# Kernel tuning notes

Measured on AMD Instinct MI355X. Metric: run time of the kernel, lower is better.

The kernel has to match this reference:

```python
import jax, jax.numpy as jnp
import numpy as np

OBS_DIM = 64
HID = 1440
K = HID // 90
N_ORN, N_PN, N_LN, N_KC, N_MBON = 24 * K, 7 * K, 4 * K, 54 * K, 1 * K
B, T, INNER = 256, 128, 4


def _lin_w(key, out_d, in_d):
    bound = 1.0 / np.sqrt(in_d)
    return jax.random.uniform(key, (out_d, in_d), jnp.float32, -bound, bound)


def setup_inputs() -> dict:
    key = jax.random.key(0)
    ks = jax.random.split(key, 20)
    return {
        "obs": jax.random.normal(ks[0], (B, T, OBS_DIM), jnp.float32),
        "h": jnp.zeros((B, HID), jnp.float32),
        "in_orn_w": _lin_w(ks[1], N_ORN, OBS_DIM),
        "in_orn_b": jnp.zeros((N_ORN,), jnp.float32),
        "W_oto": _lin_w(ks[2], N_ORN, N_ORN),
        "W_lto": _lin_w(ks[3], N_ORN, N_LN),
        "W_otp": _lin_w(ks[4], N_PN, N_ORN),
        "W_ltp": _lin_w(ks[5], N_PN, N_LN),
        "W_ptp": _lin_w(ks[6], N_PN, N_PN),
        "W_otl": _lin_w(ks[7], N_LN, N_ORN),
        "W_ptl": _lin_w(ks[8], N_LN, N_PN),
        "W_ltl": _lin_w(ks[9], N_LN, N_LN),
        "W_ktk": _lin_w(ks[10], N_KC, N_KC),
        "W_mtk": _lin_w(ks[11], N_KC, N_MBON),
        "W_ptk": _lin_w(ks[12], N_KC, N_PN),
        "W_ktm": _lin_w(ks[13], N_MBON, N_KC),
        "b_orn": jnp.zeros((N_ORN,), jnp.float32),
        "b_pn": jnp.zeros((N_PN,), jnp.float32),
        "b_ln": jnp.zeros((N_LN,), jnp.float32),
        "b_kc": jnp.zeros((N_KC,), jnp.float32),
        "b_mbon": jnp.zeros((N_MBON,), jnp.float32),
        "readout_w": _lin_w(ks[14], HID, N_MBON),
        "readout_b": jnp.zeros((HID,), jnp.float32),
    }


def reference(obs, h, in_orn_w, in_orn_b, W_oto, W_lto, W_otp, W_ltp, W_ptp,
              W_otl, W_ptl, W_ltl, W_ktk, W_mtk, W_ptk, W_ktm,
              b_orn, b_pn, b_ln, b_kc, b_mbon, readout_w, readout_b):
    # split packed hidden state into the five populations
    i0, i1, i2, i3 = N_ORN, N_ORN + N_PN, N_ORN + N_PN + N_LN, N_ORN + N_PN + N_LN + N_KC
    carry0 = (h[:, :i0], h[:, i0:i1], h[:, i1:i2], h[:, i2:i3], h[:, i3:])

    def step(h_orn, h_pn, h_ln, h_kc, h_mbon, x_t):
        orn = jnp.tanh(h_orn @ W_oto.T + h_ln @ W_lto.T + x_t + b_orn)
        pn = jnp.tanh(orn @ W_otp.T + h_ln @ W_ltp.T + h_pn @ W_ptp.T + b_pn)
        ln = jnp.tanh(orn @ W_otl.T + pn @ W_ptl.T + h_ln @ W_ltl.T + b_ln)
        kc = jnp.tanh(h_kc @ W_ktk.T + h_mbon @ W_mtk.T + pn @ W_ptk.T + b_kc)
        mbon = jnp.tanh(kc @ W_ktm.T + b_mbon)
        return orn, pn, ln, kc, mbon

    def scan_fn(carry, obs_t):  # obs_t: [B, OBS_DIM]
        x_t = obs_t @ in_orn_w.T + in_orn_b  # [B, N_ORN]
        h_orn, h_pn, h_ln, h_kc, h_mbon = carry
        for _ in range(INNER):  # fixed small inner recurrence
            h_orn, h_pn, h_ln, h_kc, h_mbon = step(h_orn, h_pn, h_ln, h_kc, h_mbon, x_t)
        y_t = h_mbon @ readout_w.T + readout_b  # [B, HID]
        return (h_orn, h_pn, h_ln, h_kc, h_mbon), y_t

    carry, ys = jax.lax.scan(scan_fn, carry0, jnp.swapaxes(obs, 0, 1))
    y = jnp.swapaxes(ys, 0, 1)  # [B, T, HID]
    h2 = jnp.concatenate(carry, axis=-1)[None]  # [1, B, HID]
    return y, h2
```

## Files before the change

kernel.cpp:

```cpp
#include <hip/hip_runtime.h>
#include <hip/hip_fp16.h>
#include <hip/hip_cooperative_groups.h>

namespace cg = cooperative_groups;

#define NTHREADS 1024
#define BT 16

constexpr int Bsz = 256, Tst = 128, HID = 1440;
constexpr int ORN = 384, PN = 112, LN = 64, KC = 864, MB = 16, OBS = 64;
constexpr int WO = 448;
constexpr int WP = 576;
constexpr int WK = 992;
constexpr int WL = 560;

struct Params {
  const float *obs, *h, *in_orn_w, *in_orn_b, *W_oto, *W_lto, *W_otp, *W_ltp, *W_ptp,
              *W_otl, *W_ptl, *W_ltl, *W_ktk, *W_mtk, *W_ptk, *W_ktm,
              *b_orn, *b_pn, *b_ln, *b_kc, *b_mbon, *readout_w, *readout_b;
  float *orn0, *orn1, *pn0, *pn1, *ln0, *ln1, *kc0, *kc1, *mbon, *y, *h2;
  __half *Wp_orn, *Wp_pn, *Wp_kc, *Wp_ln, *Wh_ktm, *Wh_ro;
  int *bar;
};

template <int K>
__device__ __forceinline__ float dot4(const float* __restrict__ w, const float* __restrict__ a) {
  const float4* w4 = (const float4*)w;
  const float4* a4 = (const float4*)a;
  float x0 = 0.f, x1 = 0.f, x2 = 0.f, x3 = 0.f;
#pragma unroll 4
  for (int i = 0; i < K / 4; ++i) {
    float4 wv = w4[i], av = a4[i];
    x0 = fmaf(wv.x, av.x, x0); x1 = fmaf(wv.y, av.y, x1);
    x2 = fmaf(wv.z, av.z, x2); x3 = fmaf(wv.w, av.w, x3);
  }
  return (x0 + x1) + (x2 + x3);
}

template <int K>
__device__ __forceinline__ float doth(const __half* __restrict__ w, const float* __restrict__ a) {
  const float4* w4 = (const float4*)w;
  const float4* a4 = (const float4*)a;
  float x0 = 0.f, x1 = 0.f, x2 = 0.f, x3 = 0.f;
#pragma unroll 4
  for (int i = 0; i < K / 8; ++i) {
    float4 wv = w4[i];
    float4 a0 = a4[2 * i], a1 = a4[2 * i + 1];
    __half2 h0 = __builtin_bit_cast(__half2, wv.x);
    __half2 h1 = __builtin_bit_cast(__half2, wv.y);
    __half2 h2 = __builtin_bit_cast(__half2, wv.z);
    __half2 h3 = __builtin_bit_cast(__half2, wv.w);
    x0 = fmaf(__low2float(h0), a0.x, x0); x1 = fmaf(__high2float(h0), a0.y, x1);
    x2 = fmaf(__low2float(h1), a0.z, x2); x3 = fmaf(__high2float(h1), a0.w, x3);
    x0 = fmaf(__low2float(h2), a1.x, x0); x1 = fmaf(__high2float(h2), a1.y, x1);
    x2 = fmaf(__low2float(h3), a1.z, x2); x3 = fmaf(__high2float(h3), a1.w, x3);
  }
  return (x0 + x1) + (x2 + x3);
}

__device__ __forceinline__ void load_seg(float* dst, int stride, int off,
                                         const float* g, int width, int b0, int tid) {
  int w4 = width >> 2;
  const float4* g4 = (const float4*)(g + (size_t)b0 * width);
  for (int idx = tid; idx < BT * w4; idx += NTHREADS) {
    int b = idx / w4, k = idx - b * w4;
    *(float4*)(dst + b * stride + off + 4 * k) = g4[(size_t)b * w4 + k];
  }
}

__device__ __forceinline__ void st_h2(__half* p, float v0, float v1) {
  __half2 h = __floats2half2_rn(v0, v1);
  __hip_atomic_store((unsigned*)p, __builtin_bit_cast(unsigned, h),
                     __ATOMIC_RELAXED, __HIP_MEMORY_SCOPE_AGENT);
}

__device__ __forceinline__ void bar_sync(int* cnt, int* gen, int& lg, int tid) {
  __syncthreads();
  if (tid == 0) {
    int target = ++lg;
    asm volatile("s_waitcnt vmcnt(0)" ::: "memory");
    int old = __hip_atomic_fetch_add(cnt, 1, __ATOMIC_RELAXED, __HIP_MEMORY_SCOPE_AGENT);
    if (old == 15) {
      __hip_atomic_store(cnt, 0, __ATOMIC_RELAXED, __HIP_MEMORY_SCOPE_AGENT);
      asm volatile("s_waitcnt vmcnt(0)" ::: "memory");
      __hip_atomic_fetch_add(gen, 1, __ATOMIC_RELAXED, __HIP_MEMORY_SCOPE_AGENT);
    } else {
      while (__hip_atomic_load(gen, __ATOMIC_RELAXED, __HIP_MEMORY_SCOPE_AGENT) < target)
        __builtin_amdgcn_s_sleep(1);
    }
    asm volatile("buffer_inv sc0\n\ts_waitcnt vmcnt(0)" ::: "memory");
  }
  __syncthreads();
}

__global__ void __launch_bounds__(NTHREADS, 4)
conn_kernel(Params P) {
  cg::grid_group grid = cg::this_grid();
  __shared__ float act[BT * 996];
  __shared__ float xs[BT * 24];
  const int tid = threadIdx.x;
  const int wg = blockIdx.x;
  const int bg = wg & 15, ng = wg >> 4, b0 = bg * BT;
  int* cnt = P.bar + bg * 64;
  int* gen = P.bar + bg * 64 + 16;
  int lg = 0;

  {
    const int gid = wg * NTHREADS + tid, gstr = 256 * NTHREADS;
    for (int idx = gid; idx < 384 * (WO / 2); idx += gstr) {
      int r = idx / (WO / 2), c = (idx - r * (WO / 2)) * 2;
      float v0, v1;
      if (c < 384) { v0 = P.W_oto[(size_t)r * 384 + c]; v1 = P.W_oto[(size_t)r * 384 + c + 1]; }
      else         { v0 = P.W_lto[(size_t)r * 64 + c - 384]; v1 = P.W_lto[(size_t)r * 64 + c - 383]; }
      st_h2(&P.Wp_orn[(size_t)r * WO + c], v0, v1);
    }
    for (int idx = gid; idx < 112 * (WP / 2); idx += gstr) {
      int r = idx / (WP / 2), c = (idx - r * (WP / 2)) * 2;
      float v0, v1;
      if      (c < 384) { v0 = P.W_otp[(size_t)r * 384 + c];     v1 = P.W_otp[(size_t)r * 384 + c + 1]; }
      else if (c < 448) { v0 = P.W_ltp[(size_t)r * 64 + c - 384]; v1 = P.W_ltp[(size_t)r * 64 + c - 383]; }
      else if (c < 560) { v0 = P.W_ptp[(size_t)r * 112 + c - 448]; v1 = P.W_ptp[(size_t)r * 112 + c - 447]; }
      else              { v0 = 0.f; v1 = 0.f; }
      st_h2(&P.Wp_pn[(size_t)r * WP + c], v0, v1);
    }
    for (int idx = gid; idx < 864 * (WK / 2); idx += gstr) {
      int r = idx / (WK / 2), c = (idx - r * (WK / 2)) * 2;
      float v0, v1;
      if      (c < 864) { v0 = P.W_ktk[(size_t)r * 864 + c];      v1 = P.W_ktk[(size_t)r * 864 + c + 1]; }
      else if (c < 976) { v0 = P.W_ptk[(size_t)r * 112 + c - 864]; v1 = P.W_ptk[(size_t)r * 112 + c - 863]; }
      else              { v0 = P.W_mtk[(size_t)r * 16 + c - 976];  v1 = P.W_mtk[(size_t)r * 16 + c - 975]; }
      st_h2(&P.Wp_kc[(size_t)r * WK + c], v0, v1);
    }
    for (int idx = gid; idx < 64 * (WL / 2); idx += gstr) {
      int r = idx / (WL / 2), c = (idx - r * (WL / 2)) * 2;
      float v0, v1;
      if      (c < 384) { v0 = P.W_otl[(size_t)r * 384 + c];      v1 = P.W_otl[(size_t)r * 384 + c + 1]; }
      else if (c < 496) { v0 = P.W_ptl[(size_t)r * 112 + c - 384]; v1 = P.W_ptl[(size_t)r * 112 + c - 383]; }
      else              { v0 = P.W_ltl[(size_t)r * 64 + c - 496];  v1 = P.W_ltl[(size_t)r * 64 + c - 495]; }
      st_h2(&P.Wp_ln[(size_t)r * WL + c], v0, v1);
    }
    for (int idx = gid; idx < 16 * 432; idx += gstr) {
      int c = idx * 2;
      st_h2(&P.Wh_ktm[c], P.W_ktm[c], P.W_ktm[c + 1]);
    }
    for (int idx = gid; idx < 1440 * 8; idx += gstr) {
      int c = idx * 2;
      st_h2(&P.Wh_ro[c], P.readout_w[c], P.readout_w[c + 1]);
    }
  }

  if (ng == 0) {
    if (tid == 0) { *cnt = 0; *gen = 0; }
    for (int idx = tid; idx < BT * HID; idx += NTHREADS) {
      int b = idx / HID, pos = idx - b * HID, gb = b0 + b;
      float v = P.h[(size_t)gb * HID + pos];
      if      (pos < 384)  P.orn1[(size_t)gb * ORN + pos] = v;
      else if (pos < 496)  P.pn1[gb * PN + (pos - 384)] = v;
      else if (pos < 560)  P.ln1[gb * LN + (pos - 496)] = v;
      else if (pos < 1424) P.kc1[(size_t)gb * KC + (pos - 560)] = v;
      else                 P.mbon[gb * MB + (pos - 1424)] = v;
    }
  }
  grid.sync();

  for (int s = 0; s < Tst * 4; ++s) {
    const int t = s >> 2, i = s & 3, p = s & 1;
    float* ornN = p ? P.orn1 : P.orn0;  const float* ornO = p ? P.orn0 : P.orn1;
    float* pnN  = p ? P.pn1  : P.pn0;   const float* pnO  = p ? P.pn0  : P.pn1;
    float* lnN  = p ? P.ln1  : P.ln0;   const float* lnO  = p ? P.ln0  : P.ln1;
    float* kcN  = p ? P.kc1  : P.kc0;   const float* kcO  = p ? P.kc0  : P.kc1;

    load_seg(act, 996, 0,   ornO, ORN, b0, tid);
    load_seg(act, 996, 384, lnO,  LN,  b0, tid);
    if (i == 0 && tid >= 640) {
      for (int o = tid - 640; o < BT * 24; o += 384) {
        int b = o / 24, jl = o - b * 24, j = ng * 24 + jl;
        xs[b * 24 + jl] = P.in_orn_b[j]
          + dot4<OBS>(P.in_orn_w + (size_t)j * OBS,
                      P.obs + ((size_t)(b0 + b) * Tst + t) * OBS);
      }
    }
    __syncthreads();
    if (tid < 384) {
      int b = tid & 15, j = tid >> 4, jg = ng * 24 + j;
      float r = xs[b * 24 + j] + P.b_orn[jg]
              + doth<WO>(P.Wp_orn + (size_t)jg * WO, act + b * 996);
      ornN[(size_t)(b0 + b) * ORN + jg] = tanhf(r);
    } else if (tid >= 448 && tid < 512 && s > 0) {
      int idx = tid - 448, b = idx >> 2, ks = idx & 3;
      float part = doth<216>(P.Wh_ktm + (size_t)ng * KC + ks * 216,
                             kcO + (size_t)(b0 + b) * KC + ks * 216);
      part += __shfl_xor(part, 1);
      part += __shfl_xor(part, 2);
      if (ks == 0)
        P.mbon[(b0 + b) * MB + ng] = tanhf(part + P.b_mbon[ng]);
    }
    bar_sync(cnt, gen, lg, tid);

    load_seg(act, 996, 0,   ornN, ORN, b0, tid);
    load_seg(act, 996, 384, lnO,  LN,  b0, tid);
    load_seg(act, 996, 448, pnO,  PN,  b0, tid);
    for (int idx = tid; idx < BT * 4; idx += NTHREADS) {
      int b = idx >> 2, k = idx & 3;
      *(float4*)(act + b * 996 + 560 + 4 * k) = make_float4(0.f, 0.f, 0.f, 0.f);
    }
    __syncthreads();
    if (tid < 448) {
      int b = tid & 15, ks = (tid >> 4) & 3, j = tid >> 6, jg = ng * 7 + j;
      float r = doth<144>(P.Wp_pn + (size_t)jg * WP + ks * 144,
                          act + b * 996 + ks * 144);
      r += __shfl_xor(r, 16);
      r += __shfl_xor(r, 32);
      if (ks == 0)
        pnN[(size_t)(b0 + b) * PN + jg] = tanhf(r + P.b_pn[jg]);
    } else if (i == 0 && s > 0 && tid >= 512) {
      for (int o = tid - 512; o < BT * 90; o += 512) {
        int b = o / 90, jl = o - b * 90, j = ng * 90 + jl;
        float yv = P.readout_b[j]
          + doth<MB>(P.Wh_ro + (size_t)j * MB, P.mbon + (size_t)(b0 + b) * MB);
        P.y[((size_t)(b0 + b) * Tst + (t - 1)) * HID + j] = yv;
      }
    }
    bar_sync(cnt, gen, lg, tid);

    load_seg(act, 996, 0,   kcO,    KC, b0, tid);
    load_seg(act, 996, 864, pnN,    PN, b0, tid);
    load_seg(act, 996, 976, P.mbon, MB, b0, tid);
    __syncthreads();
    if (tid < 864) {
      int b = tid & 15, j = tid >> 4, jg = ng * 54 + j;
      float r = P.b_kc[jg] + doth<WK>(P.Wp_kc + (size_t)jg * WK, act + b * 996);
      kcN[(size_t)(b0 + b) * KC + jg] = tanhf(r);
    } else if (tid >= 896 && tid < 960) {
      int l = tid - 896, b = l & 15, j = l >> 4, jg = ng * 4 + j;
      const __half* row = P.Wp_ln + (size_t)jg * WL;
      float r = P.b_ln[jg]
        + doth<384>(row,       ornN + (size_t)(b0 + b) * ORN)
        + doth<112>(row + 384, act + b * 996 + 864)
        + doth<64> (row + 496, lnO + (size_t)(b0 + b) * LN);
      lnN[(size_t)(b0 + b) * LN + jg] = tanhf(r);
    }
    bar_sync(cnt, gen, lg, tid);
  }

  if (tid < 64) {
    int b = tid >> 2, ks = tid & 3;
    float part = doth<216>(P.Wh_ktm + (size_t)ng * KC + ks * 216,
                           P.kc1 + (size_t)(b0 + b) * KC + ks * 216);
    part += __shfl_xor(part, 1);
    part += __shfl_xor(part, 2);
    if (ks == 0)
      P.mbon[(b0 + b) * MB + ng] = tanhf(part + P.b_mbon[ng]);
  }
  bar_sync(cnt, gen, lg, tid);
  for (int o = tid; o < BT * 90; o += NTHREADS) {
    int b = o / 90, jl = o - b * 90, j = ng * 90 + jl;
    float acc = P.readout_b[j]
      + doth<MB>(P.Wh_ro + (size_t)j * MB, P.mbon + (size_t)(b0 + b) * MB);
    P.y[((size_t)(b0 + b) * Tst + (Tst - 1)) * HID + j] = acc;
  }
  for (int idx = tid; idx < BT * 90; idx += NTHREADS) {
    int b = idx / 90, pos = idx - b * 90, gb = b0 + b;
    float v; int hp;
    if      (pos < 24) { v = P.orn1[(size_t)gb * ORN + ng * 24 + pos]; hp = ng * 24 + pos; }
    else if (pos < 31) { int l = pos - 24; v = P.pn1[gb * PN + ng * 7 + l]; hp = 384 + ng * 7 + l; }
    else if (pos < 35) { int l = pos - 31; v = P.ln1[gb * LN + ng * 4 + l]; hp = 496 + ng * 4 + l; }
    else if (pos < 89) { int l = pos - 35; v = P.kc1[(size_t)gb * KC + ng * 54 + l]; hp = 560 + ng * 54 + l; }
    else               { v = P.mbon[gb * MB + ng]; hp = 1424 + ng; }
    P.h2[(size_t)gb * HID + hp] = v;
  }
}

extern "C" void kernel_launch(void* const* d_in, const int* in_sizes, int n_in,
                              void* d_out, int out_size, void* d_ws, size_t ws_size,
                              hipStream_t stream) {
  Params P;
  P.obs       = (const float*)d_in[0];
  P.h         = (const float*)d_in[1];
  P.in_orn_w  = (const float*)d_in[2];
  P.in_orn_b  = (const float*)d_in[3];
  P.W_oto     = (const float*)d_in[4];
  P.W_lto     = (const float*)d_in[5];
  P.W_otp     = (const float*)d_in[6];
  P.W_ltp     = (const float*)d_in[7];
  P.W_ptp     = (const float*)d_in[8];
  P.W_otl     = (const float*)d_in[9];
  P.W_ptl     = (const float*)d_in[10];
  P.W_ltl     = (const float*)d_in[11];
  P.W_ktk     = (const float*)d_in[12];
  P.W_mtk     = (const float*)d_in[13];
  P.W_ptk     = (const float*)d_in[14];
  P.W_ktm     = (const float*)d_in[15];
  P.b_orn     = (const float*)d_in[16];
  P.b_pn      = (const float*)d_in[17];
  P.b_ln      = (const float*)d_in[18];
  P.b_kc      = (const float*)d_in[19];
  P.b_mbon    = (const float*)d_in[20];
  P.readout_w = (const float*)d_in[21];
  P.readout_b = (const float*)d_in[22];

  float* ws = (float*)d_ws;
  size_t off = 0;
  P.orn0 = ws + off; off += (size_t)Bsz * ORN;
  P.orn1 = ws + off; off += (size_t)Bsz * ORN;
  P.pn0  = ws + off; off += (size_t)Bsz * PN;
  P.pn1  = ws + off; off += (size_t)Bsz * PN;
  P.ln0  = ws + off; off += (size_t)Bsz * LN;
  P.ln1  = ws + off; off += (size_t)Bsz * LN;
  P.kc0  = ws + off; off += (size_t)Bsz * KC;
  P.kc1  = ws + off; off += (size_t)Bsz * KC;
  P.mbon = ws + off; off += (size_t)Bsz * MB;
  P.bar  = (int*)(ws + off); off += 16 * 64;
  P.Wp_orn = (__half*)(ws + off); off += (size_t)384 * WO / 2;
  P.Wp_pn  = (__half*)(ws + off); off += (size_t)112 * WP / 2;
  P.Wp_kc  = (__half*)(ws + off); off += (size_t)864 * WK / 2;
  P.Wp_ln  = (__half*)(ws + off); off += (size_t)64  * WL / 2;
  P.Wh_ktm = (__half*)(ws + off); off += (size_t)16  * KC / 2;
  P.Wh_ro  = (__half*)(ws + off); off += (size_t)HID * MB / 2;

  P.y  = (float*)d_out;
  P.h2 = (float*)d_out + (size_t)Bsz * Tst * HID;

  void* args[] = { &P };
  hipLaunchCooperativeKernel((void*)conn_kernel, dim3(256), dim3(NTHREADS), args, 0, stream);
}
```

Baseline: 17.60 ms.

## Store activations in fp16 and use packed fdot2 with two-row dot products

Recurrent state buffers and the shared activation tile move from fp32 to fp16, halving global and LDS traffic for the per-step state exchanges. Dot products switch to the packed v_dot2 f16 instruction, which multiplies two half pairs per instruction with an fp32 accumulator. The ORN and KC stages now compute two output rows per thread so each activation load is reused. The cost is fp16 rounding of the hidden state carried through 512 recurrent steps, which may drift numerically, and fewer active threads per stage.

```diff
diff --git a/kernel.cpp b/kernel.cpp
--- a/kernel.cpp
+++ b/kernel.cpp
@@ -13,15 +13,29 @@
 constexpr int WP = 576;
 constexpr int WK = 992;
 constexpr int WL = 560;
+constexpr int SH = 1032;
 
 struct Params {
   const float *obs, *h, *in_orn_w, *in_orn_b, *W_oto, *W_lto, *W_otp, *W_ltp, *W_ptp,
               *W_otl, *W_ptl, *W_ltl, *W_ktk, *W_mtk, *W_ptk, *W_ktm,
               *b_orn, *b_pn, *b_ln, *b_kc, *b_mbon, *readout_w, *readout_b;
-  float *orn0, *orn1, *pn0, *pn1, *ln0, *ln1, *kc0, *kc1, *mbon, *y, *h2;
+  __half *orn0, *orn1, *pn0, *pn1, *ln0, *ln1, *kc0, *kc1, *mbon;
   __half *Wp_orn, *Wp_pn, *Wp_kc, *Wp_ln, *Wh_ktm, *Wh_ro;
+  float *y, *h2;
   int *bar;
 };
+
+typedef _Float16 hv2 __attribute__((ext_vector_type(2)));
+
+__device__ __forceinline__ float fdot2u(unsigned w, unsigned a, float c) {
+#if __has_builtin(__builtin_amdgcn_fdot2)
+  return __builtin_amdgcn_fdot2(__builtin_bit_cast(hv2, w), __builtin_bit_cast(hv2, a), c, false);
+#else
+  __half2 hw = __builtin_bit_cast(__half2, w), ha = __builtin_bit_cast(__half2, a);
+  c = fmaf(__low2float(hw), __low2float(ha), c);
+  return fmaf(__high2float(hw), __high2float(ha), c);
+#endif
+}
 
 template <int K>
 __device__ __forceinline__ float dot4(const float* __restrict__ w, const float* __restrict__ a) {
@@ -38,33 +52,45 @@
 }
 
 template <int K>
-__device__ __forceinline__ float doth(const __half* __restrict__ w, const float* __restrict__ a) {
-  const float4* w4 = (const float4*)w;
-  const float4* a4 = (const float4*)a;
+__device__ __forceinline__ float doth2(const __half* __restrict__ w, const __half* __restrict__ a) {
+  const uint4* w4 = (const uint4*)w;
+  const uint4* a4 = (const uint4*)a;
   float x0 = 0.f, x1 = 0.f, x2 = 0.f, x3 = 0.f;
 #pragma unroll 4
   for (int i = 0; i < K / 8; ++i) {
-    float4 wv = w4[i];
-    float4 a0 = a4[2 * i], a1 = a4[2 * i + 1];
-    __half2 h0 = __builtin_bit_cast(__half2, wv.x);
-    __half2 h1 = __builtin_bit_cast(__half2, wv.y);
-    __half2 h2 = __builtin_bit_cast(__half2, wv.z);
-    __half2 h3 = __builtin_bit_cast(__half2, wv.w);
-    x0 = fmaf(__low2float(h0), a0.x, x0); x1 = fmaf(__high2float(h0), a0.y, x1);
-    x2 = fmaf(__low2float(h1), a0.z, x2); x3 = fmaf(__high2float(h1), a0.w, x3);
-    x0 = fmaf(__low2float(h2), a1.x, x0); x1 = fmaf(__high2float(h2), a1.y, x1);
-    x2 = fmaf(__low2float(h3), a1.z, x2); x3 = fmaf(__high2float(h3), a1.w, x3);
+    uint4 wv = w4[i], av = a4[i];
+    x0 = fdot2u(wv.x, av.x, x0); x1 = fdot2u(wv.y, av.y, x1);
+    x2 = fdot2u(wv.z, av.z, x2); x3 = fdot2u(wv.w, av.w, x3);
   }
   return (x0 + x1) + (x2 + x3);
 }
 
-__device__ __forceinline__ void load_seg(float* dst, int stride, int off,
-                                         const float* g, int width, int b0, int tid) {
-  int w4 = width >> 2;
-  const float4* g4 = (const float4*)(g + (size_t)b0 * width);
-  for (int idx = tid; idx < BT * w4; idx += NTHREADS) {
-    int b = idx / w4, k = idx - b * w4;
-    *(float4*)(dst + b * stride + off + 4 * k) = g4[(size_t)b * w4 + k];
+template <int K>
+__device__ __forceinline__ void ddoth2(const __half* __restrict__ w0, const __half* __restrict__ w1,
+                                       const __half* __restrict__ a, float& r0, float& r1) {
+  const uint4* W0 = (const uint4*)w0;
+  const uint4* W1 = (const uint4*)w1;
+  const uint4* A  = (const uint4*)a;
+  float x0=0,x1=0,x2=0,x3=0, y0=0,y1=0,y2=0,y3=0;
+#pragma unroll 4
+  for (int i = 0; i < K / 8; ++i) {
+    uint4 av = A[i], u = W0[i], v = W1[i];
+    x0 = fdot2u(u.x, av.x, x0); x1 = fdot2u(u.y, av.y, x1);
+    x2 = fdot2u(u.z, av.z, x2); x3 = fdot2u(u.w, av.w, x3);
+    y0 = fdot2u(v.x, av.x, y0); y1 = fdot2u(v.y, av.y, y1);
+    y2 = fdot2u(v.z, av.z, y2); y3 = fdot2u(v.w, av.w, y3);
+  }
+  r0 += (x0 + x1) + (x2 + x3);
+  r1 += (y0 + y1) + (y2 + y3);
+}
+
+__device__ __forceinline__ void load_seg_h(__half* dst, int offH,
+                                           const __half* g, int widthH, int b0, int tid) {
+  int w8 = widthH >> 3;
+  const uint4* g4 = (const uint4*)(g + (size_t)b0 * widthH);
+  for (int idx = tid; idx < BT * w8; idx += NTHREADS) {
+    int b = idx / w8, k = idx - b * w8;
+    *(uint4*)(dst + b * SH + offH + 8 * k) = g4[(size_t)b * w8 + k];
   }
 }
 
@@ -96,7 +122,7 @@
 __global__ void __launch_bounds__(NTHREADS, 4)
 conn_kernel(Params P) {
   cg::grid_group grid = cg::this_grid();
-  __shared__ float act[BT * 996];
+  __shared__ __align__(16) __half acth[BT * SH];
   __shared__ float xs[BT * 24];
   const int tid = threadIdx.x;
   const int wg = blockIdx.x;
@@ -153,7 +179,7 @@
     if (tid == 0) { *cnt = 0; *gen = 0; }
     for (int idx = tid; idx < BT * HID; idx += NTHREADS) {
       int b = idx / HID, pos = idx - b * HID, gb = b0 + b;
-      float v = P.h[(size_t)gb * HID + pos];
+      __half v = __float2half(P.h[(size_t)gb * HID + pos]);
       if      (pos < 384)  P.orn1[(size_t)gb * ORN + pos] = v;
       else if (pos < 496)  P.pn1[gb * PN + (pos - 384)] = v;
       else if (pos < 560)  P.ln1[gb * LN + (pos - 496)] = v;
@@ -165,13 +191,13 @@
 
   for (int s = 0; s < Tst * 4; ++s) {
     const int t = s >> 2, i = s & 3, p = s & 1;
-    float* ornN = p ? P.orn1 : P.orn0;  const float* ornO = p ? P.orn0 : P.orn1;
-    float* pnN  = p ? P.pn1  : P.pn0;   const float* pnO  = p ? P.pn0  : P.pn1;
-    float* lnN  = p ? P.ln1  : P.ln0;   const float* lnO  = p ? P.ln0  : P.ln1;
-    float* kcN  = p ? P.kc1  : P.kc0;   const float* kcO  = p ? P.kc0  : P.kc1;
-
-    load_seg(act, 996, 0,   ornO, ORN, b0, tid);
-    load_seg(act, 996, 384, lnO,  LN,  b0, tid);
+    __half* ornN = p ? P.orn1 : P.orn0;  const __half* ornO = p ? P.orn0 : P.orn1;
+    __half* pnN  = p ? P.pn1  : P.pn0;   const __half* pnO  = p ? P.pn0  : P.pn1;
+    __half* lnN  = p ? P.ln1  : P.ln0;   const __half* lnO  = p ? P.ln0  : P.ln1;
+    __half* kcN  = p ? P.kc1  : P.kc0;   const __half* kcO  = p ? P.kc0  : P.kc1;
+
+    load_seg_h(acth, 0,   ornO, ORN, b0, tid);
+    load_seg_h(acth, 384, lnO,  LN,  b0, tid);
     if (i == 0 && tid >= 640) {
       for (int o = tid - 640; o < BT * 24; o += 384) {
         int b = o / 24, jl = o - b * 24, j = ng * 24 + jl;
@@ -181,92 +207,98 @@
       }
     }
     __syncthreads();
-    if (tid < 384) {
-      int b = tid & 15, j = tid >> 4, jg = ng * 24 + j;
-      float r = xs[b * 24 + j] + P.b_orn[jg]
-              + doth<WO>(P.Wp_orn + (size_t)jg * WO, act + b * 996);
-      ornN[(size_t)(b0 + b) * ORN + jg] = tanhf(r);
-    } else if (tid >= 448 && tid < 512 && s > 0) {
-      int idx = tid - 448, b = idx >> 2, ks = idx & 3;
-      float part = doth<216>(P.Wh_ktm + (size_t)ng * KC + ks * 216,
-                             kcO + (size_t)(b0 + b) * KC + ks * 216);
+    if (tid < 192) {
+      int b = tid & 15, jp = tid >> 4;
+      int j0 = ng * 24 + 2 * jp, j1 = j0 + 1;
+      float r0 = xs[b * 24 + 2 * jp]     + P.b_orn[j0];
+      float r1 = xs[b * 24 + 2 * jp + 1] + P.b_orn[j1];
+      ddoth2<WO>(P.Wp_orn + (size_t)j0 * WO, P.Wp_orn + (size_t)j1 * WO,
+                 acth + b * SH, r0, r1);
+      *(__half2*)&ornN[(size_t)(b0 + b) * ORN + j0] = __floats2half2_rn(tanhf(r0), tanhf(r1));
+    } else if (tid < 256 && s > 0) {
+      int idx = tid - 192, b = idx >> 2, ks = idx & 3;
+      float part = doth2<216>(P.Wh_ktm + (size_t)ng * KC + ks * 216,
+                              kcO + (size_t)(b0 + b) * KC + ks * 216);
       part += __shfl_xor(part, 1);
       part += __shfl_xor(part, 2);
       if (ks == 0)
-        P.mbon[(b0 + b) * MB + ng] = tanhf(part + P.b_mbon[ng]);
+        P.mbon[(b0 + b) * MB + ng] = __float2half(tanhf(part + P.b_mbon[ng]));
     }
     bar_sync(cnt, gen, lg, tid);
 
-    load_seg(act, 996, 0,   ornN, ORN, b0, tid);
-    load_seg(act, 996, 384, lnO,  LN,  b0, tid);
-    load_seg(act, 996, 448, pnO,  PN,  b0, tid);
-    for (int idx = tid; idx < BT * 4; idx += NTHREADS) {
-      int b = idx >> 2, k = idx & 3;
-      *(float4*)(act + b * 996 + 560 + 4 * k) = make_float4(0.f, 0.f, 0.f, 0.f);
+    load_seg_h(acth, 0,   ornN, ORN, b0, tid);
+    load_seg_h(acth, 384, lnO,  LN,  b0, tid);
+    load_seg_h(acth, 448, pnO,  PN,  b0, tid);
+    for (int idx = tid; idx < BT * 2; idx += NTHREADS) {
+      int b = idx >> 1, k = idx & 1;
+      *(uint4*)(acth + b * SH + 560 + 8 * k) = make_uint4(0, 0, 0, 0);
     }
     __syncthreads();
     if (tid < 448) {
       int b = tid & 15, ks = (tid >> 4) & 3, j = tid >> 6, jg = ng * 7 + j;
-      float r = doth<144>(P.Wp_pn + (size_t)jg * WP + ks * 144,
-                          act + b * 996 + ks * 144);
+      float r = doth2<144>(P.Wp_pn + (size_t)jg * WP + ks * 144,
+                           acth + b * SH + ks * 144);
       r += __shfl_xor(r, 16);
       r += __shfl_xor(r, 32);
       if (ks == 0)
-        pnN[(size_t)(b0 + b) * PN + jg] = tanhf(r + P.b_pn[jg]);
+        pnN[(size_t)(b0 + b) * PN + jg] = __float2half(tanhf(r + P.b_pn[jg]));
     } else if (i == 0 && s > 0 && tid >= 512) {
       for (int o = tid - 512; o < BT * 90; o += 512) {
         int b = o / 90, jl = o - b * 90, j = ng * 90 + jl;
         float yv = P.readout_b[j]
-          + doth<MB>(P.Wh_ro + (size_t)j * MB, P.mbon + (size_t)(b0 + b) * MB);
+          + doth2<MB>(P.Wh_ro + (size_t)j * MB, P.mbon + (size_t)(b0 + b) * MB);
         P.y[((size_t)(b0 + b) * Tst + (t - 1)) * HID + j] = yv;
       }
     }
     bar_sync(cnt, gen, lg, tid);
 
-    load_seg(act, 996, 0,   kcO,    KC, b0, tid);
-    load_seg(act, 996, 864, pnN,    PN, b0, tid);
-    load_seg(act, 996, 976, P.mbon, MB, b0, tid);
+    load_seg_h(acth, 0,   kcO,    KC, b0, tid);
+    load_seg_h(acth, 864, pnN,    PN, b0, tid);
+    load_seg_h(acth, 976, P.mbon, MB, b0, tid);
     __syncthreads();
-    if (tid < 864) {
-      int b = tid & 15, j = tid >> 4, jg = ng * 54 + j;
-      float r = P.b_kc[jg] + doth<WK>(P.Wp_kc + (size_t)jg * WK, act + b * 996);
-      kcN[(size_t)(b0 + b) * KC + jg] = tanhf(r);
-    } else if (tid >= 896 && tid < 960) {
-      int l = tid - 896, b = l & 15, j = l >> 4, jg = ng * 4 + j;
+    if (tid < 432) {
+      int b = tid & 15, jp = tid >> 4;
+      int j0 = ng * 54 + 2 * jp, j1 = j0 + 1;
+      float r0 = P.b_kc[j0], r1 = P.b_kc[j1];
+      ddoth2<WK>(P.Wp_kc + (size_t)j0 * WK, P.Wp_kc + (size_t)j1 * WK,
+                 acth + b * SH, r0, r1);
+      *(__half2*)&kcN[(size_t)(b0 + b) * KC + j0] = __floats2half2_rn(tanhf(r0), tanhf(r1));
+    } else if (tid >= 448 && tid < 512) {
+      int l = tid - 448, b = l & 15, j = l >> 4, jg = ng * 4 + j;
       const __half* row = P.Wp_ln + (size_t)jg * WL;
       float r = P.b_ln[jg]
-        + doth<384>(row,       ornN + (size_t)(b0 + b) * ORN)
-        + doth<112>(row + 384, act + b * 996 + 864)
-        + doth<64> (row + 496, lnO + (size_t)(b0 + b) * LN);
-      lnN[(size_t)(b0 + b) * LN + jg] = tanhf(r);
+        + doth2<384>(row,       ornN + (size_t)(b0 + b) * ORN)
+        + doth2<112>(row + 384, acth + b * SH + 864)
+        + doth2<64> (row + 496, lnO + (size_t)(b0 + b) * LN);
+      lnN[(size_t)(b0 + b) * LN + jg] = __float2half(tanhf(r));
     }
     bar_sync(cnt, gen, lg, tid);
   }
 
   if (tid < 64) {
     int b = tid >> 2, ks = tid & 3;
-    float part = doth<216>(P.Wh_ktm + (size_t)ng * KC + ks * 216,
-                           P.kc1 + (size_t)(b0 + b) * KC + ks * 216);
+    float part = doth2<216>(P.Wh_ktm + (size_t)ng * KC + ks * 216,
+                            P.kc1 + (size_t)(b0 + b) * KC + ks * 216);
     part += __shfl_xor(part, 1);
     part += __shfl_xor(part, 2);
     if (ks == 0)
-      P.mbon[(b0 + b) * MB + ng] = tanhf(part + P.b_mbon[ng]);
+      P.mbon[(b0 + b) * MB + ng] = __float2half(tanhf(part + P.b_mbon[ng]));
   }
   bar_sync(cnt, gen, lg, tid);
   for (int o = tid; o < BT * 90; o += NTHREADS) {
     int b = o / 90, jl = o - b * 90, j = ng * 90 + jl;
     float acc = P.readout_b[j]
-      + doth<MB>(P.Wh_ro + (size_t)j * MB, P.mbon + (size_t)(b0 + b) * MB);
+      + doth2<MB>(P.Wh_ro + (size_t)j * MB, P.mbon + (size_t)(b0 + b) * MB);
     P.y[((size_t)(b0 + b) * Tst + (Tst - 1)) * HID + j] = acc;
   }
   for (int idx = tid; idx < BT * 90; idx += NTHREADS) {
     int b = idx / 90, pos = idx - b * 90, gb = b0 + b;
     float v; int hp;
-    if      (pos < 24) { v = P.orn1[(size_t)gb * ORN + ng * 24 + pos]; hp = ng * 24 + pos; }
-    else if (pos < 31) { int l = pos - 24; v = P.pn1[gb * PN + ng * 7 + l]; hp = 384 + ng * 7 + l; }
-    else if (pos < 35) { int l = pos - 31; v = P.ln1[gb * LN + ng * 4 + l]; hp = 496 + ng * 4 + l; }
-    else if (pos < 89) { int l = pos - 35; v = P.kc1[(size_t)gb * KC + ng * 54 + l]; hp = 560 + ng * 54 + l; }
-    else               { v = P.mbon[gb * MB + ng]; hp = 1424 + ng; }
+    if      (pos < 24) { v = __half2float(P.orn1[(size_t)gb * ORN + ng * 24 + pos]); hp = ng * 24 + pos; }
+    else if (pos < 31) { int l = pos - 24; v = __half2float(P.pn1[gb * PN + ng * 7 + l]); hp = 384 + ng * 7 + l; }
+    else if (pos < 35) { int l = pos - 31; v = __half2float(P.ln1[gb * LN + ng * 4 + l]); hp = 496 + ng * 4 + l; }
+    else if (pos < 89) { int l = pos - 35; v = __half2float(P.kc1[(size_t)gb * KC + ng * 54 + l]); hp = 560 + ng * 54 + l; }
+    else               { v = __half2float(P.mbon[gb * MB + ng]); hp = 1424 + ng; }
     P.h2[(size_t)gb * HID + hp] = v;
   }
 }
@@ -299,24 +331,24 @@
   P.readout_w = (const float*)d_in[21];
   P.readout_b = (const float*)d_in[22];
 
-  float* ws = (float*)d_ws;
+  __half* wh = (__half*)d_ws;
   size_t off = 0;
-  P.orn0 = ws + off; off += (size_t)Bsz * ORN;
-  P.orn1 = ws + off; off += (size_t)Bsz * ORN;
-  P.pn0  = ws + off; off += (size_t)Bsz * PN;
-  P.pn1  = ws + off; off += (size_t)Bsz * PN;
-  P.ln0  = ws + off; off += (size_t)Bsz * LN;
-  P.ln1  = ws + off; off += (size_t)Bsz * LN;
-  P.kc0  = ws + off; off += (size_t)Bsz * KC;
-  P.kc1  = ws + off; off += (size_t)Bsz * KC;
-  P.mbon = ws + off; off += (size_t)Bsz * MB;
-  P.bar  = (int*)(ws + off); off += 16 * 64;
-  P.Wp_orn = (__half*)(ws + off); off += (size_t)384 * WO / 2;
-  P.Wp_pn  = (__half*)(ws + off); off += (size_t)112 * WP / 2;
-  P.Wp_kc  = (__half*)(ws + off); off += (size_t)864 * WK / 2;
-  P.Wp_ln  = (__half*)(ws + off); off += (size_t)64  * WL / 2;
-  P.Wh_ktm = (__half*)(ws + off); off += (size_t)16  * KC / 2;
-  P.Wh_ro  = (__half*)(ws + off); off += (size_t)HID * MB / 2;
+  P.orn0 = wh + off; off += (size_t)Bsz * ORN;
+  P.orn1 = wh + off; off += (size_t)Bsz * ORN;
+  P.pn0  = wh + off; off += (size_t)Bsz * PN;
+  P.pn1  = wh + off; off += (size_t)Bsz * PN;
+  P.ln0  = wh + off; off += (size_t)Bsz * LN;
+  P.ln1  = wh + off; off += (size_t)Bsz * LN;
+  P.kc0  = wh + off; off += (size_t)Bsz * KC;
+  P.kc1  = wh + off; off += (size_t)Bsz * KC;
+  P.mbon = wh + off; off += (size_t)Bsz * MB;
+  P.bar  = (int*)(wh + off); off += 16 * 64 * 2;
+  P.Wp_orn = wh + off; off += (size_t)384 * WO;
+  P.Wp_pn  = wh + off; off += (size_t)112 * WP;
+  P.Wp_kc  = wh + off; off += (size_t)864 * WK;
+  P.Wp_ln  = wh + off; off += (size_t)64  * WL;
+  P.Wh_ktm = wh + off; off += (size_t)16  * KC;
+  P.Wh_ro  = wh + off; off += (size_t)HID * MB;
 
   P.y  = (float*)d_out;
   P.h2 = (float*)d_out + (size_t)Bsz * Tst * HID;
```

Result: faster. 16.82 ms (-4.4%).
